# Performance work log

Hardware: AMD Instinct MI355X
Metric: run time of the kernel (lower is better)

## Reference

```python
import jax, jax.numpy as jnp
import numpy as np

EPS = 1e-8  # torch F.cosine_similarity default eps


def setup_inputs() -> dict:
    key = jax.random.key(0)
    k1, k2, k3 = jax.random.split(key, 3)
    B, D, C = 65536, 512, 10000
    embeddings = jax.random.normal(k1, (B, D), dtype=jnp.float32)
    labels = jax.random.randint(k2, (B,), 0, C, dtype=jnp.int64)
    prototypes = jax.random.normal(k3, (C, D), dtype=jnp.float32)
    return {"embeddings": embeddings, "labels": labels, "prototypes": prototypes}


def reference(embeddings, labels, prototypes):
    # Batched gather of per-sample prototypes: [B, D]
    protos = prototypes[labels]
    # Cosine similarity per sample (torch eps semantics: clamp norm at eps)
    e_norm = jnp.maximum(jnp.linalg.norm(embeddings, axis=-1), EPS)
    p_norm = jnp.maximum(jnp.linalg.norm(protos, axis=-1), EPS)
    cos = jnp.sum(embeddings * protos, axis=-1) / (e_norm * p_norm)
    return 1.0 - jnp.mean(cos)
```

## Files before the change

kernel.cpp:

```cpp
#include <hip/hip_runtime.h>
#include <math.h>

#define COS_EPS 1e-8f

typedef float vfloat4 __attribute__((ext_vector_type(4)));

__device__ __forceinline__ float dot4(vfloat4 a, vfloat4 b) {
    return fmaf(a.x, b.x, fmaf(a.y, b.y, fmaf(a.z, b.z, a.w * b.w)));
}

__global__ __launch_bounds__(256) void assignment_loss_kernel(
    const float* __restrict__ emb,
    const int*   __restrict__ labels,
    const float* __restrict__ protos,
    float*       __restrict__ part,
    int B, int D)
{
    const int lane = threadIdx.x & 63;
    const int grp  = lane >> 4;
    const int gl   = lane & 15;
    const int wib  = threadIdx.x >> 6;
    const int wpb  = blockDim.x >> 6;
    const int gw   = blockIdx.x * wpb + wib;
    const int nw   = gridDim.x * wpb;

    float local = 0.0f;

    if (D == 512 && (B % (4 * nw)) == 0) {
        const int iters = B / (4 * nw);
        int s   = gw * 4 + grp;
        int lbl = labels[s];

        for (int i = 0; i < iters; ++i) {
            const int s_next   = s + 4 * nw;
            const int lbl_next = (i + 1 < iters) ? labels[s_next] : 0;

            const vfloat4* e = (const vfloat4*)(emb    + (size_t)s   * 512);
            const vfloat4* p = (const vfloat4*)(protos + (size_t)lbl * 512);

            vfloat4 ev[8], pv[8];
            #pragma unroll
            for (int c = 0; c < 8; ++c) ev[c] = __builtin_nontemporal_load(&e[c * 16 + gl]);
            #pragma unroll
            for (int c = 0; c < 8; ++c) pv[c] = p[c * 16 + gl];

            float dot = 0.f, esq = 0.f, psq = 0.f;
            #pragma unroll
            for (int c = 0; c < 8; ++c) {
                dot += dot4(ev[c], pv[c]);
                esq += dot4(ev[c], ev[c]);
                psq += dot4(pv[c], pv[c]);
            }

            #pragma unroll
            for (int off = 8; off > 0; off >>= 1) {
                dot += __shfl_xor(dot, off, 64);
                esq += __shfl_xor(esq, off, 64);
                psq += __shfl_xor(psq, off, 64);
            }

            if (gl == 0) {
                float en = fmaxf(sqrtf(esq), COS_EPS);
                float pn = fmaxf(sqrtf(psq), COS_EPS);
                local += dot / (en * pn);
            }

            s = s_next; lbl = lbl_next;
        }
    } else {
        const int nchunks = D >> 8;
        for (int smp = gw; smp < B; smp += nw) {
            const int l = labels[smp];
            const vfloat4* e = (const vfloat4*)(emb    + (size_t)smp * (size_t)D);
            const vfloat4* p = (const vfloat4*)(protos + (size_t)l   * (size_t)D);
            float dot = 0.f, esq = 0.f, psq = 0.f;
            for (int c = 0; c < nchunks; ++c) {
                vfloat4 ev = __builtin_nontemporal_load(&e[c * 64 + lane]);
                vfloat4 pv = p[c * 64 + lane];
                dot += dot4(ev, pv);
                esq += dot4(ev, ev);
                psq += dot4(pv, pv);
            }
            #pragma unroll
            for (int off = 32; off > 0; off >>= 1) {
                dot += __shfl_xor(dot, off, 64);
                esq += __shfl_xor(esq, off, 64);
                psq += __shfl_xor(psq, off, 64);
            }
            if (lane == 0) {
                float en = fmaxf(sqrtf(esq), COS_EPS);
                float pn = fmaxf(sqrtf(psq), COS_EPS);
                local += dot / (en * pn);
            }
        }
    }

    #pragma unroll
    for (int off = 32; off > 0; off >>= 1) local += __shfl_xor(local, off, 64);

    __shared__ float smem[8];
    if (lane == 0) smem[wib] = local;
    __syncthreads();
    if (threadIdx.x == 0) {
        float bs = 0.0f;
        for (int w = 0; w < wpb; ++w) bs += smem[w];
        part[blockIdx.x] = bs;
    }
}

__global__ __launch_bounds__(256) void assignment_loss_finalize(
    const float* __restrict__ part,
    float*       __restrict__ out,
    int nparts, float invB)
{
    float s = 0.0f;
    for (int i = threadIdx.x; i < nparts; i += 256) s += part[i];
    #pragma unroll
    for (int off = 32; off > 0; off >>= 1) s += __shfl_xor(s, off, 64);

    __shared__ float smem[4];
    const int lane = threadIdx.x & 63;
    const int wib  = threadIdx.x >> 6;
    if (lane == 0) smem[wib] = s;
    __syncthreads();
    if (threadIdx.x == 0) {
        float t = smem[0] + smem[1] + smem[2] + smem[3];
        out[0] = 1.0f - t * invB;
    }
}

extern "C" void kernel_launch(void* const* d_in, const int* in_sizes, int n_in,
                              void* d_out, int out_size, void* d_ws, size_t ws_size,
                              hipStream_t stream) {
    const float* emb    = (const float*)d_in[0];
    const int*   labels = (const int*)  d_in[1];
    const float* protos = (const float*)d_in[2];
    float*       out    = (float*)d_out;
    float*       part   = (float*)d_ws;

    const int B = in_sizes[1];
    const int D = in_sizes[0] / B;

    const int block = 256;
    const int grid  = 1024;
    assignment_loss_kernel<<<grid, block, 0, stream>>>(emb, labels, protos, part, B, D);
    assignment_loss_finalize<<<1, block, 0, stream>>>(part, out, grid, 1.0f / (float)B);
}
```

Measured before the change: 204.8 us.

## Sort samples by label via counting sort before cosine loss

Adds histogram, prefix-scan and scatter kernels that build a label-sorted permutation of the samples, and processes samples in that order. Each warp then handles contiguous runs of the same label, so prototype rows are reused from cache. This adds four extra launches, atomics and a single-block scan, and turns the embedding reads into permuted row gathers.

```diff
diff --git a/kernel.cpp b/kernel.cpp
--- a/kernel.cpp
+++ b/kernel.cpp
@@ -9,10 +9,61 @@
     return fmaf(a.x, b.x, fmaf(a.y, b.y, fmaf(a.z, b.z, a.w * b.w)));
 }
 
+
+__global__ __launch_bounds__(256) void hist_kernel(
+    const int* __restrict__ labels, int* __restrict__ hist, int B)
+{
+    int i = blockIdx.x * blockDim.x + threadIdx.x;
+    if (i < B) atomicAdd(&hist[labels[i]], 1);
+}
+
+__global__ __launch_bounds__(1024) void scan_kernel(int* __restrict__ hist, int C)
+{
+    __shared__ int smem[1024];
+    const int t = threadIdx.x;
+    const int chunk = (C + 1023) >> 10;
+    const int lo = t * chunk;
+    const int hi = (lo + chunk < C) ? lo + chunk : C;
+
+    int sum = 0;
+    for (int i = lo; i < hi; ++i) sum += hist[i];
+    smem[t] = sum;
+    __syncthreads();
+
+    for (int off = 1; off < 1024; off <<= 1) {
+        int v = 0;
+        if (t >= off) v = smem[t - off];
+        __syncthreads();
+        if (t >= off) smem[t] += v;
+        __syncthreads();
+    }
+
+    int run = (t > 0) ? smem[t - 1] : 0;
+    for (int i = lo; i < hi; ++i) {
+        int v = hist[i];
+        hist[i] = run;
+        run += v;
+    }
+}
+
+__global__ __launch_bounds__(256) void scatter_kernel(
+    const int* __restrict__ labels, int* __restrict__ offs,
+    int* __restrict__ perm, int* __restrict__ slbl, int B)
+{
+    int i = blockIdx.x * blockDim.x + threadIdx.x;
+    if (i < B) {
+        int l = labels[i];
+        int pos = atomicAdd(&offs[l], 1);
+        perm[pos] = i;
+        slbl[pos] = l;
+    }
+}
+
 __global__ __launch_bounds__(256) void assignment_loss_kernel(
     const float* __restrict__ emb,
-    const int*   __restrict__ labels,
     const float* __restrict__ protos,
+    const int*   __restrict__ perm,
+    const int*   __restrict__ slbl,
     float*       __restrict__ part,
     int B, int D)
 {
@@ -27,13 +78,16 @@
     float local = 0.0f;
 
     if (D == 512 && (B % (4 * nw)) == 0) {
-        const int iters = B / (4 * nw);
-        int s   = gw * 4 + grp;
-        int lbl = labels[s];
+        const int spw   = B / nw;
+        const int iters = spw >> 2;
+        int j   = gw * spw + grp;
+        int s   = perm[j];
+        int lbl = slbl[j];
 
         for (int i = 0; i < iters; ++i) {
-            const int s_next   = s + 4 * nw;
-            const int lbl_next = (i + 1 < iters) ? labels[s_next] : 0;
+            const int j_next = j + 4;
+            int s_next = 0, lbl_next = 0;
+            if (i + 1 < iters) { s_next = perm[j_next]; lbl_next = slbl[j_next]; }
 
             const vfloat4* e = (const vfloat4*)(emb    + (size_t)s   * 512);
             const vfloat4* p = (const vfloat4*)(protos + (size_t)lbl * 512);
@@ -65,12 +119,13 @@
                 local += dot / (en * pn);
             }
 
-            s = s_next; lbl = lbl_next;
+            j = j_next; s = s_next; lbl = lbl_next;
         }
     } else {
         const int nchunks = D >> 8;
-        for (int smp = gw; smp < B; smp += nw) {
-            const int l = labels[smp];
+        for (int jj = gw; jj < B; jj += nw) {
+            const int smp = perm[jj];
+            const int l   = slbl[jj];
             const vfloat4* e = (const vfloat4*)(emb    + (size_t)smp * (size_t)D);
             const vfloat4* p = (const vfloat4*)(protos + (size_t)l   * (size_t)D);
             float dot = 0.f, esq = 0.f, psq = 0.f;
@@ -136,13 +191,25 @@
     const int*   labels = (const int*)  d_in[1];
     const float* protos = (const float*)d_in[2];
     float*       out    = (float*)d_out;
-    float*       part   = (float*)d_ws;
 
     const int B = in_sizes[1];
     const int D = in_sizes[0] / B;
+    const int C = in_sizes[2] / D;
+
+    int*   hist = (int*)d_ws;
+    int*   perm = hist + C;
+    int*   slbl = perm + B;
+    float* part = (float*)(slbl + B);
+
+    hipMemsetAsync(hist, 0, (size_t)C * sizeof(int), stream);
 
     const int block = 256;
-    const int grid  = 1024;
-    assignment_loss_kernel<<<grid, block, 0, stream>>>(emb, labels, protos, part, B, D);
+    const int bgrid = (B + block - 1) / block;
+    hist_kernel   <<<bgrid, block, 0, stream>>>(labels, hist, B);
+    scan_kernel   <<<1, 1024, 0, stream>>>(hist, C);
+    scatter_kernel<<<bgrid, block, 0, stream>>>(labels, hist, perm, slbl, B);
+
+    const int grid = 1024;
+    assignment_loss_kernel<<<grid, block, 0, stream>>>(emb, protos, perm, slbl, part, B, D);
     assignment_loss_finalize<<<1, block, 0, stream>>>(part, out, grid, 1.0f / (float)B);
 }
```

Measured after the change: 225.1 us. 9.9% more time.
